# Performance work log

Hardware: AMD Instinct MI355X
Metric: run time of the kernel (lower is better)

The kernel has to match this reference:

```python
import jax, jax.numpy as jnp
import numpy as np
import math

B, N, D = 512, 256, 128

def setup_inputs() -> dict:
    key = jax.random.key(0)
    ks = jax.random.split(key, 7)
    mirror_nodes = jax.random.normal(ks[0], (B, N, D), dtype=jnp.float32)
    satellite_nodes = jax.random.normal(ks[1], (B, N, D), dtype=jnp.float32)
    mask = jax.random.randint(ks[2], (B, N), 0, 2).astype(bool)
    mask = mask.at[:, 0].set(True)  # ensure at least one valid key per row
    Wq1 = jax.random.normal(ks[3], (D, D), dtype=jnp.float32) / math.sqrt(D)
    Wk1 = jax.random.normal(ks[4], (D, D), dtype=jnp.float32) / math.sqrt(D)
    Wq2 = jax.random.normal(ks[5], (D, D), dtype=jnp.float32) / math.sqrt(D)
    Wk2 = jax.random.normal(ks[6], (D, D), dtype=jnp.float32) / math.sqrt(D)
    return {"mirror_nodes": mirror_nodes, "satellite_nodes": satellite_nodes,
            "satellite_node_mask": mask, "Wq1": Wq1, "Wk1": Wk1, "Wq2": Wq2, "Wk2": Wk2}

def reference(mirror_nodes, satellite_nodes, satellite_node_mask, Wq1, Wk1, Wq2, Wk2):
    dim = mirror_nodes.shape[-1]
    scale = 1.0 / math.sqrt(dim)
    # per-node gate: <Wq1 s_i, Wk1 m_i> / sqrt(d)  -> [B, N, 1]
    q1 = jnp.einsum('bnd,ed->bne', satellite_nodes, Wq1)
    k1 = jnp.einsum('bnd,ed->bne', mirror_nodes, Wk1)
    alpha = (jnp.einsum('bne,bne->bn', q1, k1) * scale)[:, :, None]
    sat_out = satellite_nodes + alpha * (mirror_nodes - satellite_nodes)
    # attention over satellites: beta [B, N, N]
    q2 = jnp.einsum('bnd,ed->bne', mirror_nodes, Wq2)
    k2 = jnp.einsum('bnd,ed->bne', sat_out, Wk2)
    beta = jnp.einsum('bie,bje->bij', q2, k2) * scale
    beta = jnp.where(satellite_node_mask[:, None, :], beta, -jnp.inf)
    beta = jax.nn.softmax(beta, axis=2)
    mir_out = jnp.einsum('bij,bjd->bid', beta, mirror_nodes)
    return (sat_out, mir_out)
```

## Files before the change

kernel.cpp:

```cpp
#include <hip/hip_runtime.h>
#include <hip/hip_bf16.h>

typedef unsigned int u32;
typedef unsigned short u16;
typedef __attribute__((ext_vector_type(8))) short short8v;
typedef __attribute__((ext_vector_type(4))) float f32x4;

#define BB 512
#define NN 256
#define DD 128
#define SCALE 0.08838834764831845f

__device__ __forceinline__ float bf2f(u16 u) {
  union { u32 i; float f; } v; v.i = ((u32)u) << 16; return v.f;
}
__device__ __forceinline__ u16 f2bf(float f) {
  union { u32 i; float f; } v; v.f = f;
  u32 i = v.i;
  u32 rounded = i + 0x7FFFu + ((i >> 16) & 1u);
  return (u16)(rounded >> 16);
}
__device__ __forceinline__ u32 pack2(float a, float b) {
  return (u32)f2bf(a) | ((u32)f2bf(b) << 16);
}

#define SWZ(row, byteInRow)  ((((row) * 256) + (byteInRow)) ^ (((row) & 7) << 4))
#define SWZT(row, byteInRow) ((((row) * 512) + (byteInRow)) ^ (((row) & 7) << 4))

__global__ void k_prep(const float* __restrict__ Wq1, const float* __restrict__ Wk1,
                       const float* __restrict__ Wq2, const float* __restrict__ Wk2,
                       u16* __restrict__ Mbf) {
  int d = blockIdx.x & 127;
  bool first = blockIdx.x < 128;
  const float* Wq = first ? Wq1 : Wq2;
  const float* Wk = first ? Wk1 : Wk2;
  u16* out = Mbf + (first ? 0 : 16384);
  int dp = threadIdx.x;
  float acc = 0.f;
  for (int e = 0; e < 128; ++e)
    acc += Wq[e * 128 + d] * Wk[e * 128 + dp];
  out[d * 128 + dp] = f2bf(acc);
}

__global__ __launch_bounds__(512, 2) void k_stage1(
    const float* __restrict__ mir, const float* __restrict__ sat,
    const u16* __restrict__ Mbf, float* __restrict__ out0, float* __restrict__ out1) {
  __shared__ char soB[32768];
  int tid = threadIdx.x;
  int lane = tid & 63, w = tid >> 6;
  int rA = lane & 15;
  int g = lane >> 4;
  int base = blockIdx.x * 128 + w * 16;
  const u16* M1bf = Mbf;
  const u16* M2bf = Mbf + 16384;
  char* wbuf = soB + w * 4096;

  short8v amir[4];
#pragma unroll
  for (int kk = 0; kk < 4; ++kk) {
    const float* p = mir + (size_t)(base + rA) * 128 + kk * 32 + g * 8;
    float4 f0 = *(const float4*)p;
    float4 f1 = *(const float4*)(p + 4);
    union { short8v s; u32 u[4]; } uu;
    uu.u[0] = pack2(f0.x, f0.y); uu.u[1] = pack2(f0.z, f0.w);
    uu.u[2] = pack2(f1.x, f1.y); uu.u[3] = pack2(f1.z, f1.w);
    amir[kk] = uu.s;
  }
  f32x4 acc1[8];
#pragma unroll
  for (int et = 0; et < 8; ++et) {
    acc1[et] = (f32x4)(0.f);
#pragma unroll
    for (int kk = 0; kk < 4; ++kk) {
      short8v bf = *(const short8v*)(M1bf + (et * 16 + rA) * 128 + kk * 32 + g * 8);
      acc1[et] = __builtin_amdgcn_mfma_f32_16x16x32_bf16(amir[kk], bf, acc1[et], 0, 0, 0);
    }
  }
  float sval[8][4], mval[8][4];
#pragma unroll
  for (int r = 0; r < 4; ++r) {
    size_t n = (size_t)base + g * 4 + r;
#pragma unroll
    for (int et = 0; et < 8; ++et) {
      sval[et][r] = sat[n * 128 + et * 16 + rA];
      mval[et][r] = mir[n * 128 + et * 16 + rA];
    }
  }
  float alph[4];
#pragma unroll
  for (int r = 0; r < 4; ++r) {
    float p = 0.f;
#pragma unroll
    for (int et = 0; et < 8; ++et) p += acc1[et][r] * sval[et][r];
    p += __shfl_xor(p, 1, 64);
    p += __shfl_xor(p, 2, 64);
    p += __shfl_xor(p, 4, 64);
    p += __shfl_xor(p, 8, 64);
    alph[r] = p * SCALE;
  }
#pragma unroll
  for (int r = 0; r < 4; ++r) {
    size_t n = (size_t)base + g * 4 + r;
#pragma unroll
    for (int et = 0; et < 8; ++et) {
      float so = sval[et][r] + alph[r] * (mval[et][r] - sval[et][r]);
      out0[n * 128 + et * 16 + rA] = so;
      *(u16*)(wbuf + SWZ(g * 4 + r, (et * 16 + rA) * 2)) = f2bf(so);
    }
  }
  short8v aso[4];
#pragma unroll
  for (int kk = 0; kk < 4; ++kk)
    aso[kk] = *(const short8v*)(wbuf + SWZ(rA, kk * 64 + g * 16));
  f32x4 acc2[8];
#pragma unroll
  for (int et = 0; et < 8; ++et) {
    acc2[et] = (f32x4)(0.f);
#pragma unroll
    for (int kk = 0; kk < 4; ++kk) {
      short8v bf = *(const short8v*)(M2bf + (et * 16 + rA) * 128 + kk * 32 + g * 8);
      acc2[et] = __builtin_amdgcn_mfma_f32_16x16x32_bf16(aso[kk], bf, acc2[et], 0, 0, 0);
    }
  }
#pragma unroll
  for (int r = 0; r < 4; ++r) {
    size_t n = (size_t)base + g * 4 + r;
#pragma unroll
    for (int et = 0; et < 8; ++et)
      out1[n * 128 + et * 16 + rA] = acc2[et][r];
  }
}

__global__ __launch_bounds__(512, 2) void k_attn(
    const float* __restrict__ mir, const int* __restrict__ mask,
    float* __restrict__ out1) {
  extern __shared__ char smem[];
  char* k2Bc = smem;
  char* mirBc = smem + 65536;
  int* maskS = (int*)(smem + 131072);

  int b = blockIdx.x, tid = threadIdx.x;
  int lane = tid & 63, w = tid >> 6;
  int rA = lane & 15;
  int g = lane >> 4;

  const float2* k2g = (const float2*)(out1 + (size_t)b * 32768);
  const float2* mirg = (const float2*)(mir + (size_t)b * 32768);
  for (int idx = tid; idx < 16384; idx += 512) {
    int j = idx >> 6, c = idx & 63;
    float2 kf = k2g[idx];
    *(u32*)(k2Bc + SWZ(j, c * 4)) = pack2(kf.x, kf.y);
    float2 mf = mirg[idx];
    *(u32*)(mirBc + SWZ(j, c * 4)) = pack2(mf.x, mf.y);
  }
  if (tid < 256) maskS[tid] = mask[b * 256 + tid];
  __syncthreads();

  f32x4 acc[16][2];
#pragma unroll
  for (int jt = 0; jt < 16; ++jt)
#pragma unroll
    for (int it = 0; it < 2; ++it) acc[jt][it] = (f32x4)(0.f);
#pragma unroll
  for (int kk = 0; kk < 4; ++kk) {
    int kb = (kk * 32 + g * 8) * 2;
    short8v bfr[2];
#pragma unroll
    for (int it = 0; it < 2; ++it)
      bfr[it] = *(const short8v*)(mirBc + SWZ(32 * w + it * 16 + rA, kb));
#pragma unroll
    for (int jt = 0; jt < 16; ++jt) {
      short8v afr = *(const short8v*)(k2Bc + SWZ(jt * 16 + rA, kb));
#pragma unroll
      for (int it = 0; it < 2; ++it)
        acc[jt][it] = __builtin_amdgcn_mfma_f32_16x16x32_bf16(afr, bfr[it], acc[jt][it], 0, 0, 0);
    }
  }
  __syncthreads();

  {
    const float* mirf = mir + (size_t)b * 32768;
    int d = tid & 127, jb = tid >> 7;
    for (int i2 = 0; i2 < 32; ++i2) {
      int j2 = jb + 4 * i2;
      float a0 = mirf[(size_t)(2 * j2) * 128 + d];
      float a1 = mirf[(size_t)(2 * j2 + 1) * 128 + d];
      *(u32*)(k2Bc + SWZT(d, j2 * 4)) = pack2(a0, a1);
    }
  }

#pragma unroll
  for (int it = 0; it < 2; ++it) {
    float mx = -1e30f;
#pragma unroll
    for (int jt = 0; jt < 16; ++jt)
#pragma unroll
      for (int r = 0; r < 4; ++r) {
        int j = jt * 16 + g * 4 + r;
        float s = maskS[j] ? acc[jt][it][r] * SCALE : -1e30f;
        acc[jt][it][r] = s;
        mx = fmaxf(mx, s);
      }
    mx = fmaxf(mx, __shfl_xor(mx, 16, 64));
    mx = fmaxf(mx, __shfl_xor(mx, 32, 64));
    float sum = 0.f;
#pragma unroll
    for (int jt = 0; jt < 16; ++jt)
#pragma unroll
      for (int r = 0; r < 4; ++r) {
        float e = __expf(acc[jt][it][r] - mx);
        acc[jt][it][r] = e;
        sum += e;
      }
    sum += __shfl_xor(sum, 16, 64);
    sum += __shfl_xor(sum, 32, 64);
    float inv = 1.f / sum;
#pragma unroll
    for (int jt = 0; jt < 16; ++jt)
#pragma unroll
      for (int r = 0; r < 4; ++r) acc[jt][it][r] *= inv;
  }
  __syncthreads();

  char* Pw = mirBc + w * 8192;
  f32x4 oacc[2][8];
#pragma unroll
  for (int it = 0; it < 2; ++it)
#pragma unroll
    for (int dt = 0; dt < 8; ++dt) oacc[it][dt] = (f32x4)(0.f);

  for (int h = 0; h < 2; ++h) {
#pragma unroll
    for (int it = 0; it < 2; ++it)
#pragma unroll
      for (int jt8 = 0; jt8 < 8; ++jt8) {
        int jt = 8 * h + jt8;
#pragma unroll
        for (int r = 0; r < 4; ++r) {
          int iLoc = it * 16 + rA;
          int jh = jt8 * 16 + g * 4 + r;
          *(u16*)(Pw + SWZ(iLoc, jh * 2)) = f2bf(acc[jt][it][r]);
        }
      }
#pragma unroll
    for (int kk2 = 0; kk2 < 4; ++kk2) {
      int kbP = (kk2 * 32 + g * 8) * 2;
      int kbT = (128 * h + kk2 * 32 + g * 8) * 2;
      short8v pa[2];
#pragma unroll
      for (int it = 0; it < 2; ++it)
        pa[it] = *(const short8v*)(Pw + SWZ(it * 16 + rA, kbP));
#pragma unroll
      for (int dt = 0; dt < 8; ++dt) {
        short8v vb = *(const short8v*)(k2Bc + SWZT(dt * 16 + rA, kbT));
#pragma unroll
        for (int it = 0; it < 2; ++it)
          oacc[it][dt] = __builtin_amdgcn_mfma_f32_16x16x32_bf16(pa[it], vb, oacc[it][dt], 0, 0, 0);
      }
    }
  }

#pragma unroll
  for (int it = 0; it < 2; ++it)
#pragma unroll
    for (int dt = 0; dt < 8; ++dt)
#pragma unroll
      for (int r = 0; r < 4; ++r) {
        int iG = 32 * w + it * 16 + g * 4 + r;
        int dG = dt * 16 + rA;
        out1[((size_t)b * 256 + iG) * 128 + dG] = oacc[it][dt][r];
      }
}

extern "C" void kernel_launch(void* const* d_in, const int* in_sizes, int n_in,
                              void* d_out, int out_size, void* d_ws, size_t ws_size,
                              hipStream_t stream) {
  const float* mir = (const float*)d_in[0];
  const float* sat = (const float*)d_in[1];
  const int* mask = (const int*)d_in[2];
  const float* Wq1 = (const float*)d_in[3];
  const float* Wk1 = (const float*)d_in[4];
  const float* Wq2 = (const float*)d_in[5];
  const float* Wk2 = (const float*)d_in[6];
  float* out0 = (float*)d_out;
  float* out1 = out0 + (size_t)BB * NN * DD;
  u16* Mbf = (u16*)d_ws;

  hipFuncSetAttribute((const void*)k_attn, hipFuncAttributeMaxDynamicSharedMemorySize, 132096);

  k_prep<<<256, 128, 0, stream>>>(Wq1, Wk1, Wq2, Wk2, Mbf);
  k_stage1<<<1024, 512, 0, stream>>>(mir, sat, Mbf, out0, out1);
  k_attn<<<512, 512, 132096, stream>>>(mir, mask, out1);
}
```

Baseline: 351.2 us.

## Fuse gating and key projection stage into attention kernel

Merges the per-node gate and K2 projection kernel into the attention kernel so each block computes k2 for its batch directly into shared memory in bf16. This removes the fp32 k2 write to and re-read from global memory, and one kernel launch. In exchange, the projection work now runs at the attention kernel's low occupancy of one large-shared-memory block per batch.

```diff
diff --git a/kernel.cpp b/kernel.cpp
--- a/kernel.cpp
+++ b/kernel.cpp
@@ -42,118 +42,116 @@
   out[d * 128 + dp] = f2bf(acc);
 }
 
-__global__ __launch_bounds__(512, 2) void k_stage1(
+__global__ __launch_bounds__(512, 2) void k_fused(
     const float* __restrict__ mir, const float* __restrict__ sat,
-    const u16* __restrict__ Mbf, float* __restrict__ out0, float* __restrict__ out1) {
-  __shared__ char soB[32768];
-  int tid = threadIdx.x;
-  int lane = tid & 63, w = tid >> 6;
-  int rA = lane & 15;
-  int g = lane >> 4;
-  int base = blockIdx.x * 128 + w * 16;
-  const u16* M1bf = Mbf;
-  const u16* M2bf = Mbf + 16384;
-  char* wbuf = soB + w * 4096;
-
-  short8v amir[4];
-#pragma unroll
-  for (int kk = 0; kk < 4; ++kk) {
-    const float* p = mir + (size_t)(base + rA) * 128 + kk * 32 + g * 8;
-    float4 f0 = *(const float4*)p;
-    float4 f1 = *(const float4*)(p + 4);
-    union { short8v s; u32 u[4]; } uu;
-    uu.u[0] = pack2(f0.x, f0.y); uu.u[1] = pack2(f0.z, f0.w);
-    uu.u[2] = pack2(f1.x, f1.y); uu.u[3] = pack2(f1.z, f1.w);
-    amir[kk] = uu.s;
-  }
-  f32x4 acc1[8];
-#pragma unroll
-  for (int et = 0; et < 8; ++et) {
-    acc1[et] = (f32x4)(0.f);
-#pragma unroll
-    for (int kk = 0; kk < 4; ++kk) {
-      short8v bf = *(const short8v*)(M1bf + (et * 16 + rA) * 128 + kk * 32 + g * 8);
-      acc1[et] = __builtin_amdgcn_mfma_f32_16x16x32_bf16(amir[kk], bf, acc1[et], 0, 0, 0);
-    }
-  }
-  float sval[8][4], mval[8][4];
-#pragma unroll
-  for (int r = 0; r < 4; ++r) {
-    size_t n = (size_t)base + g * 4 + r;
-#pragma unroll
-    for (int et = 0; et < 8; ++et) {
-      sval[et][r] = sat[n * 128 + et * 16 + rA];
-      mval[et][r] = mir[n * 128 + et * 16 + rA];
-    }
-  }
-  float alph[4];
-#pragma unroll
-  for (int r = 0; r < 4; ++r) {
-    float p = 0.f;
-#pragma unroll
-    for (int et = 0; et < 8; ++et) p += acc1[et][r] * sval[et][r];
-    p += __shfl_xor(p, 1, 64);
-    p += __shfl_xor(p, 2, 64);
-    p += __shfl_xor(p, 4, 64);
-    p += __shfl_xor(p, 8, 64);
-    alph[r] = p * SCALE;
-  }
-#pragma unroll
-  for (int r = 0; r < 4; ++r) {
-    size_t n = (size_t)base + g * 4 + r;
-#pragma unroll
-    for (int et = 0; et < 8; ++et) {
-      float so = sval[et][r] + alph[r] * (mval[et][r] - sval[et][r]);
-      out0[n * 128 + et * 16 + rA] = so;
-      *(u16*)(wbuf + SWZ(g * 4 + r, (et * 16 + rA) * 2)) = f2bf(so);
-    }
-  }
-  short8v aso[4];
-#pragma unroll
-  for (int kk = 0; kk < 4; ++kk)
-    aso[kk] = *(const short8v*)(wbuf + SWZ(rA, kk * 64 + g * 16));
-  f32x4 acc2[8];
-#pragma unroll
-  for (int et = 0; et < 8; ++et) {
-    acc2[et] = (f32x4)(0.f);
-#pragma unroll
-    for (int kk = 0; kk < 4; ++kk) {
-      short8v bf = *(const short8v*)(M2bf + (et * 16 + rA) * 128 + kk * 32 + g * 8);
-      acc2[et] = __builtin_amdgcn_mfma_f32_16x16x32_bf16(aso[kk], bf, acc2[et], 0, 0, 0);
-    }
-  }
-#pragma unroll
-  for (int r = 0; r < 4; ++r) {
-    size_t n = (size_t)base + g * 4 + r;
-#pragma unroll
-    for (int et = 0; et < 8; ++et)
-      out1[n * 128 + et * 16 + rA] = acc2[et][r];
-  }
-}
-
-__global__ __launch_bounds__(512, 2) void k_attn(
-    const float* __restrict__ mir, const int* __restrict__ mask,
-    float* __restrict__ out1) {
+    const int* __restrict__ mask, const u16* __restrict__ Mbf,
+    float* __restrict__ out0, float* __restrict__ out1) {
   extern __shared__ char smem[];
-  char* k2Bc = smem;
-  char* mirBc = smem + 65536;
+  char* reg0 = smem;
+  char* reg1 = smem + 65536;
   int* maskS = (int*)(smem + 131072);
 
   int b = blockIdx.x, tid = threadIdx.x;
   int lane = tid & 63, w = tid >> 6;
   int rA = lane & 15;
   int g = lane >> 4;
-
-  const float2* k2g = (const float2*)(out1 + (size_t)b * 32768);
+  const u16* M1bf = Mbf;
+  const u16* M2bf = Mbf + 16384;
+
   const float2* mirg = (const float2*)(mir + (size_t)b * 32768);
   for (int idx = tid; idx < 16384; idx += 512) {
     int j = idx >> 6, c = idx & 63;
-    float2 kf = k2g[idx];
-    *(u32*)(k2Bc + SWZ(j, c * 4)) = pack2(kf.x, kf.y);
     float2 mf = mirg[idx];
-    *(u32*)(mirBc + SWZ(j, c * 4)) = pack2(mf.x, mf.y);
+    *(u32*)(reg1 + SWZ(j, c * 4)) = pack2(mf.x, mf.y);
   }
   if (tid < 256) maskS[tid] = mask[b * 256 + tid];
+  __syncthreads();
+
+  f32x4 acc1[2][8];
+#pragma unroll
+  for (int it = 0; it < 2; ++it)
+#pragma unroll
+    for (int et = 0; et < 8; ++et) acc1[it][et] = (f32x4)(0.f);
+#pragma unroll
+  for (int kk = 0; kk < 4; ++kk) {
+    int kb = (kk * 32 + g * 8) * 2;
+    short8v am[2];
+#pragma unroll
+    for (int it = 0; it < 2; ++it)
+      am[it] = *(const short8v*)(reg1 + SWZ(32 * w + it * 16 + rA, kb));
+#pragma unroll
+    for (int et = 0; et < 8; ++et) {
+      short8v bf = *(const short8v*)(M1bf + (et * 16 + rA) * 128 + kk * 32 + g * 8);
+#pragma unroll
+      for (int it = 0; it < 2; ++it)
+        acc1[it][et] = __builtin_amdgcn_mfma_f32_16x16x32_bf16(am[it], bf, acc1[it][et], 0, 0, 0);
+    }
+  }
+
+  size_t gbase = (size_t)b * 256 + 32 * w;
+#pragma unroll
+  for (int it = 0; it < 2; ++it) {
+    float sv[8][4], mv[8][4];
+#pragma unroll
+    for (int r = 0; r < 4; ++r) {
+      size_t n = gbase + it * 16 + g * 4 + r;
+#pragma unroll
+      for (int et = 0; et < 8; ++et) {
+        sv[et][r] = sat[n * 128 + et * 16 + rA];
+        mv[et][r] = mir[n * 128 + et * 16 + rA];
+      }
+    }
+#pragma unroll
+    for (int r = 0; r < 4; ++r) {
+      float p = 0.f;
+#pragma unroll
+      for (int et = 0; et < 8; ++et) p += acc1[it][et][r] * sv[et][r];
+      p += __shfl_xor(p, 1, 64);
+      p += __shfl_xor(p, 2, 64);
+      p += __shfl_xor(p, 4, 64);
+      p += __shfl_xor(p, 8, 64);
+      float al = p * SCALE;
+      size_t n = gbase + it * 16 + g * 4 + r;
+      int jloc = 32 * w + it * 16 + g * 4 + r;
+#pragma unroll
+      for (int et = 0; et < 8; ++et) {
+        float so = sv[et][r] + al * (mv[et][r] - sv[et][r]);
+        out0[n * 128 + et * 16 + rA] = so;
+        *(u16*)(reg0 + SWZ(jloc, (et * 16 + rA) * 2)) = f2bf(so);
+      }
+    }
+  }
+
+  short8v aso[2][4];
+#pragma unroll
+  for (int it = 0; it < 2; ++it)
+#pragma unroll
+    for (int kk = 0; kk < 4; ++kk)
+      aso[it][kk] = *(const short8v*)(reg0 + SWZ(32 * w + it * 16 + rA, (kk * 32 + g * 8) * 2));
+  f32x4 acc2[2][8];
+#pragma unroll
+  for (int it = 0; it < 2; ++it)
+#pragma unroll
+    for (int et = 0; et < 8; ++et) acc2[it][et] = (f32x4)(0.f);
+#pragma unroll
+  for (int kk = 0; kk < 4; ++kk) {
+#pragma unroll
+    for (int et = 0; et < 8; ++et) {
+      short8v bf = *(const short8v*)(M2bf + (et * 16 + rA) * 128 + kk * 32 + g * 8);
+#pragma unroll
+      for (int it = 0; it < 2; ++it)
+        acc2[it][et] = __builtin_amdgcn_mfma_f32_16x16x32_bf16(aso[it][kk], bf, acc2[it][et], 0, 0, 0);
+    }
+  }
+#pragma unroll
+  for (int it = 0; it < 2; ++it)
+#pragma unroll
+    for (int r = 0; r < 4; ++r) {
+      int jloc = 32 * w + it * 16 + g * 4 + r;
+#pragma unroll
+      for (int et = 0; et < 8; ++et)
+        *(u16*)(reg0 + SWZ(jloc, (et * 16 + rA) * 2)) = f2bf(acc2[it][et][r]);
+    }
   __syncthreads();
 
   f32x4 acc[16][2];
@@ -167,10 +165,10 @@
     short8v bfr[2];
 #pragma unroll
     for (int it = 0; it < 2; ++it)
-      bfr[it] = *(const short8v*)(mirBc + SWZ(32 * w + it * 16 + rA, kb));
+      bfr[it] = *(const short8v*)(reg1 + SWZ(32 * w + it * 16 + rA, kb));
 #pragma unroll
     for (int jt = 0; jt < 16; ++jt) {
-      short8v afr = *(const short8v*)(k2Bc + SWZ(jt * 16 + rA, kb));
+      short8v afr = *(const short8v*)(reg0 + SWZ(jt * 16 + rA, kb));
 #pragma unroll
       for (int it = 0; it < 2; ++it)
         acc[jt][it] = __builtin_amdgcn_mfma_f32_16x16x32_bf16(afr, bfr[it], acc[jt][it], 0, 0, 0);
@@ -185,7 +183,7 @@
       int j2 = jb + 4 * i2;
       float a0 = mirf[(size_t)(2 * j2) * 128 + d];
       float a1 = mirf[(size_t)(2 * j2 + 1) * 128 + d];
-      *(u32*)(k2Bc + SWZT(d, j2 * 4)) = pack2(a0, a1);
+      *(u32*)(reg0 + SWZT(d, j2 * 4)) = pack2(a0, a1);
     }
   }
 
@@ -222,7 +220,7 @@
   }
   __syncthreads();
 
-  char* Pw = mirBc + w * 8192;
+  char* Pw = reg1 + w * 8192;
   f32x4 oacc[2][8];
 #pragma unroll
   for (int it = 0; it < 2; ++it)
@@ -252,7 +250,7 @@
         pa[it] = *(const short8v*)(Pw + SWZ(it * 16 + rA, kbP));
 #pragma unroll
       for (int dt = 0; dt < 8; ++dt) {
-        short8v vb = *(const short8v*)(k2Bc + SWZT(dt * 16 + rA, kbT));
+        short8v vb = *(const short8v*)(reg0 + SWZT(dt * 16 + rA, kbT));
 #pragma unroll
         for (int it = 0; it < 2; ++it)
           oacc[it][dt] = __builtin_amdgcn_mfma_f32_16x16x32_bf16(pa[it], vb, oacc[it][dt], 0, 0, 0);
@@ -286,9 +284,8 @@
   float* out1 = out0 + (size_t)BB * NN * DD;
   u16* Mbf = (u16*)d_ws;
 
-  hipFuncSetAttribute((const void*)k_attn, hipFuncAttributeMaxDynamicSharedMemorySize, 132096);
+  hipFuncSetAttribute((const void*)k_fused, hipFuncAttributeMaxDynamicSharedMemorySize, 132096);
 
   k_prep<<<256, 128, 0, stream>>>(Wq1, Wk1, Wq2, Wk2, Mbf);
-  k_stage1<<<1024, 512, 0, stream>>>(mir, sat, Mbf, out0, out1);
-  k_attn<<<512, 512, 132096, stream>>>(mir, mask, out1);
-}
+  k_fused<<<512, 512, 132096, stream>>>(mir, sat, mask, Mbf, out0, out1);
+}
```

Result: faster. 322.7 us (-8.1%).
